# Optimization experiments

Hardware: AMD Instinct MI355X
Metric: run time of the kernel (lower is better)

## Reference

```python
import jax, jax.numpy as jnp
import numpy as np

D = 256          # embed_dim
NS = 400000      # num_symbols
PAD = NS         # padding index
B = 2048         # query batch
FEW = 5          # support set size
K = 64           # max neighbors
DM = 2 * D       # d_model
DI = 2 * DM      # ffn inner dim
H = 2 * DM       # lstm hidden
STEPS = 4        # process_steps
EPS = 1e-3       # LayerNormalization eps


def setup_inputs():
    key = jax.random.key(0)
    ks = jax.random.split(key, 20)
    emb = (jax.random.normal(ks[0], (NS + 1, D), jnp.float32) * 0.02).at[PAD].set(0.0)
    gcn_W = jax.random.normal(ks[1], (D, 2 * D), jnp.float32) * (1.0 / np.sqrt(2 * D))
    gcn_wb = jnp.zeros((D,), jnp.float32)
    gcn_b = jnp.zeros((D,), jnp.float32)
    gate_w = 1.0 + jax.random.normal(ks[2], (NS, 1), jnp.float32) * 0.05
    gate_temp = jnp.asarray(1.0, jnp.float32)
    p1_W = jax.random.normal(ks[3], (DI, DM), jnp.float32) * (1.0 / np.sqrt(DM))
    p1_b = jnp.zeros((DI,), jnp.float32)
    p2_W = jax.random.normal(ks[4], (DM, DI), jnp.float32) * (1.0 / np.sqrt(DI))
    p2_b = jnp.zeros((DM,), jnp.float32)
    ln_a = jnp.ones((DM,), jnp.float32)
    ln_b = jnp.zeros((DM,), jnp.float32)
    W_ih = jax.random.normal(ks[5], (4 * H, DM), jnp.float32) * (1.0 / np.sqrt(DM))
    W_hh = jax.random.normal(ks[6], (4 * H, H), jnp.float32) * (1.0 / np.sqrt(H))
    b_ih = jnp.zeros((4 * H,), jnp.float32)
    b_hh = jnp.zeros((4 * H,), jnp.float32)
    query = jax.random.randint(ks[7], (B, 2), 0, NS)
    support = jax.random.randint(ks[8], (FEW, 2), 0, NS)
    q_l1 = jax.random.randint(ks[9], (B, K, 2), 0, NS)
    q_deg_l = jax.random.randint(ks[10], (B,), 0, K + 1)
    q_r1 = jax.random.randint(ks[11], (B, K, 2), 0, NS)
    q_deg_r = jax.random.randint(ks[12], (B,), 0, K + 1)
    s_l1 = jax.random.randint(ks[13], (FEW, K, 2), 0, NS)
    s_deg_l = jax.random.randint(ks[14], (FEW,), 0, K + 1)
    s_r1 = jax.random.randint(ks[15], (FEW, K, 2), 0, NS)
    s_deg_r = jax.random.randint(ks[16], (FEW,), 0, K + 1)
    return dict(emb=emb, gcn_W=gcn_W, gcn_wb=gcn_wb, gcn_b=gcn_b, gate_w=gate_w,
                gate_temp=gate_temp, p1_W=p1_W, p1_b=p1_b, p2_W=p2_W, p2_b=p2_b,
                ln_a=ln_a, ln_b=ln_b, W_ih=W_ih, W_hh=W_hh, b_ih=b_ih, b_hh=b_hh,
                query=query, support=support, q_l1=q_l1, q_deg_l=q_deg_l,
                q_r1=q_r1, q_deg_r=q_deg_r, s_l1=s_l1, s_deg_l=s_deg_l,
                s_r1=s_r1, s_deg_r=s_deg_r)


def _neighbor_encoder(emb, gcn_W, gcn_wb, gcn_b, gate_w, gate_temp, conn, deg, self_ids):
    rel = conn[:, :, 0]                                       # [N, K]
    ent = conn[:, :, 1]
    cat = jnp.concatenate([emb[rel], emb[ent]], axis=-1)      # [N, K, 2D]
    proj = jax.nn.leaky_relu(jnp.einsum('nkc,dc->nkd', cat, gcn_W) + gcn_wb + gcn_b)
    proj = jnp.where((rel == PAD)[:, :, None], 0.0, proj)     # zero out pad neighbors
    degf = deg.astype(jnp.float32)
    agg = proj.sum(axis=1) / jnp.maximum(degf, 1.0)[:, None]  # masked mean over K
    nrel = jnp.where(rel == PAD, 0, rel)
    gate = jax.nn.sigmoid(gate_w[nrel, 0].mean(axis=1, keepdims=True) / gate_temp)
    gate = jnp.where(degf[:, None] > 0, gate, 1.0)
    return jnp.tanh(emb[self_ids] + gate * agg)               # [N, D]


def _layer_norm(z, a, b):
    mu = z.mean(axis=-1, keepdims=True)
    sigma = jnp.std(z, axis=-1, keepdims=True, ddof=1)        # torch.std is unbiased
    return (z - mu) / (sigma + EPS) * a + b


def _support_encoder(x, p1_W, p1_b, p2_W, p2_b, ln_a, ln_b):
    h = jax.nn.relu(x @ p1_W.T + p1_b)
    return _layer_norm(h @ p2_W.T + p2_b + x, ln_a, ln_b)


def _query_encoder(support, query, W_ih, W_hh, b_ih, b_hh):
    n = query.shape[0]
    h_r = jnp.zeros((n, H), query.dtype)
    c = jnp.zeros((n, H), query.dtype)
    h = query
    for _ in range(STEPS):  # small fixed process-step loop
        gates = query @ W_ih.T + b_ih + h_r @ W_hh.T + b_hh
        i, f, g, o = jnp.split(gates, 4, axis=1)
        c = jax.nn.sigmoid(f) * c + jax.nn.sigmoid(i) * jnp.tanh(g)
        h_new = jax.nn.sigmoid(o) * jnp.tanh(c)
        h = query + h_new[:, :DM]
        attn = jax.nn.softmax(h @ support.T, axis=1)
        h_r = jnp.concatenate([h, attn @ support], axis=1)
    return h


def reference(emb, gcn_W, gcn_wb, gcn_b, gate_w, gate_temp, p1_W, p1_b, p2_W, p2_b,
              ln_a, ln_b, W_ih, W_hh, b_ih, b_hh,
              query, support, q_l1, q_deg_l, q_r1, q_deg_r, s_l1, s_deg_l, s_r1, s_deg_r):
    ne = lambda conn, deg, ids: _neighbor_encoder(emb, gcn_W, gcn_wb, gcn_b, gate_w,
                                                  gate_temp, conn, deg, ids)
    q_vec = jnp.concatenate([ne(q_l1, q_deg_l, query[:, 0]),
                             ne(q_r1, q_deg_r, query[:, 1])], axis=-1)   # [B, 2D]
    s_vec = jnp.concatenate([ne(s_l1, s_deg_l, support[:, 0]),
                             ne(s_r1, s_deg_r, support[:, 1])], axis=-1) # [FEW, 2D]
    s_g = _support_encoder(s_vec, p1_W, p1_b, p2_W, p2_b, ln_a, ln_b).mean(axis=0, keepdims=True)
    q_enc = _support_encoder(q_vec, p1_W, p1_b, p2_W, p2_b, ln_a, ln_b)
    q_g = _query_encoder(s_g, q_enc, W_ih, W_hh, b_ih, b_hh)
    return jnp.sum(q_g * s_g, axis=1)                                     # [B]
```

## Files before the change

kernel.cpp:

```cpp
#include <hip/hip_runtime.h>
#include <math.h>

#define PADID 400000

typedef __attribute__((ext_vector_type(8))) short bf16x8;
typedef __attribute__((ext_vector_type(4))) float f32x4;

__device__ __forceinline__ float sigmoidf_(float x){ return 1.0f/(1.0f+__expf(-x)); }
__device__ __forceinline__ float ftanh(float x){ return 1.0f - 2.0f/(__expf(2.0f*x)+1.0f); }

__device__ __forceinline__ unsigned short f2bf(float f){
    unsigned u = __float_as_uint(f);
    u += 0x7FFFu + ((u >> 16) & 1u);
    return (unsigned short)(u >> 16);
}
__device__ __forceinline__ float bf2f(unsigned short s){
    return __uint_as_float(((unsigned)s) << 16);
}

__device__ __forceinline__ int perm_orig(int mp){
    int gate = (mp >> 4) & 3;
    int j = (mp >> 6) * 16 + (mp & 15);
    return gate * 1024 + j;
}

__global__ __launch_bounds__(256) void preconvert(
    const float* __restrict__ gcnW, const float* __restrict__ p1W,
    const float* __restrict__ p2W, const float* __restrict__ Wih,
    const float* __restrict__ Whh, const float* __restrict__ b_ih,
    const float* __restrict__ b_hh,
    unsigned short* __restrict__ wgcn, unsigned short* __restrict__ p1w,
    unsigned short* __restrict__ p2w, unsigned short* __restrict__ wih_p,
    unsigned short* __restrict__ whh_p, float* __restrict__ bias0_p)
{
    long long i = ((long long)blockIdx.x * 256 + threadIdx.x) * 4;
    float4 v;
    if (i < 131072LL) {
        v = *(const float4*)(gcnW + i);
        unsigned a0 = f2bf(v.x) | ((unsigned)f2bf(v.y) << 16);
        unsigned a1 = f2bf(v.z) | ((unsigned)f2bf(v.w) << 16);
        *(uint2*)(wgcn + i) = make_uint2(a0, a1);
    } else if (i < 655360LL) {
        long long off = i - 131072LL;
        v = *(const float4*)(p1W + off);
        unsigned a0 = f2bf(v.x) | ((unsigned)f2bf(v.y) << 16);
        unsigned a1 = f2bf(v.z) | ((unsigned)f2bf(v.w) << 16);
        *(uint2*)(p1w + off) = make_uint2(a0, a1);
    } else if (i < 1179648LL) {
        long long off = i - 655360LL;
        v = *(const float4*)(p2W + off);
        unsigned a0 = f2bf(v.x) | ((unsigned)f2bf(v.y) << 16);
        unsigned a1 = f2bf(v.z) | ((unsigned)f2bf(v.w) << 16);
        *(uint2*)(p2w + off) = make_uint2(a0, a1);
    } else if (i < 3276800LL) {
        long long off = i - 1179648LL;
        int mp = (int)(off >> 9), col = (int)(off & 511);
        int orig = perm_orig(mp);
        v = *(const float4*)(Wih + (long long)orig * 512 + col);
        unsigned a0 = f2bf(v.x) | ((unsigned)f2bf(v.y) << 16);
        unsigned a1 = f2bf(v.z) | ((unsigned)f2bf(v.w) << 16);
        *(uint2*)(wih_p + off) = make_uint2(a0, a1);
    } else if (i < 5373952LL) {
        long long off = i - 3276800LL;
        int mp = (int)(off >> 9), col = (int)(off & 511);
        int orig = perm_orig(mp);
        v = *(const float4*)(Whh + (long long)orig * 1024 + col);
        unsigned a0 = f2bf(v.x) | ((unsigned)f2bf(v.y) << 16);
        unsigned a1 = f2bf(v.z) | ((unsigned)f2bf(v.w) << 16);
        *(uint2*)(whh_p + off) = make_uint2(a0, a1);
    } else if (i < 5378048LL) {
        long long off = i - 5373952LL;
        #pragma unroll
        for (int q = 0; q < 4; q++) {
            int mp = (int)off + q;
            int orig = perm_orig(mp);
            bias0_p[mp] = b_ih[orig] + b_hh[orig];
        }
    }
}

__device__ __forceinline__ void ne_decode(int s,
    const int* q_l1, const int* q_deg_l, const int* q_r1, const int* q_deg_r,
    const int* s_l1, const int* s_deg_l, const int* s_r1, const int* s_deg_r,
    const int* query, const int* support,
    const int*& conn, const int*& deg, const int*& ids, int& n, int& ids_off, int& row, int& col)
{
    if (s < 2048)      { conn = q_l1; deg = q_deg_l; ids = query;   n = s;      ids_off = 0; row = s;        col = 0;   }
    else if (s < 4096) { conn = q_r1; deg = q_deg_r; ids = query;   n = s-2048; ids_off = 1; row = s-2048;   col = 256; }
    else if (s < 4101) { conn = s_l1; deg = s_deg_l; ids = support; n = s-4096; ids_off = 0; row = 2048+n;   col = 0;   }
    else               { conn = s_r1; deg = s_deg_r; ids = support; n = s-4101; ids_off = 1; row = 2048+n;   col = 256; }
}

__global__ __launch_bounds__(256, 2) void ne_fused(
    const float* __restrict__ emb, const unsigned short* __restrict__ Wbf,
    const float* __restrict__ wb, const float* __restrict__ bb,
    const float* __restrict__ gate_w, const float* __restrict__ gate_temp,
    const int* __restrict__ q_l1, const int* __restrict__ q_deg_l,
    const int* __restrict__ q_r1, const int* __restrict__ q_deg_r,
    const int* __restrict__ s_l1, const int* __restrict__ s_deg_l,
    const int* __restrict__ s_r1, const int* __restrict__ s_deg_r,
    const int* __restrict__ query, const int* __restrict__ support,
    unsigned short* __restrict__ vec_bf)
{
    __shared__ int   rel_s[128];
    __shared__ int   ent_s[128];
    __shared__ unsigned short A_lds[128 * 72];
    __shared__ unsigned short B_lds[256 * 72];
    __shared__ float red[4][4][128];
    __shared__ float gw_s[128];
    __shared__ float gate_sh[2];

    const int bid = blockIdx.x;
    const int t = threadIdx.x;
    const int lane = t & 63, w = t >> 6, lr = lane & 15, kg = lane >> 4;
    const int si_w = w >> 1;
    const int wc0 = (w & 1) * 128;

    {
        int si = t >> 7, u = t & 127;
        const int *conn, *deg, *ids; int n, ids_off, row, col;
        ne_decode(bid*2 + si, q_l1,q_deg_l,q_r1,q_deg_r,s_l1,s_deg_l,s_r1,s_deg_r,
                  query, support, conn, deg, ids, n, ids_off, row, col);
        int v = conn[n*128 + u];
        if (u & 1) ent_s[si*64 + (u>>1)] = v; else rel_s[si*64 + (u>>1)] = v;
    }
    __syncthreads();

    const int rr = t >> 1, half = t & 1;

    float4 a_reg[8];
    #define ISSUE_A(ch_) { \
        const int side_ = ((ch_) >= 4); \
        const int cg0_ = ((ch_) & 3) * 64; \
        int rowid_ = side_ ? ent_s[rr] : rel_s[rr]; \
        const float* src_ = emb + (long long)rowid_ * 256 + cg0_ + half * 32; \
        _Pragma("unroll") \
        for (int q_ = 0; q_ < 8; q_++) a_reg[q_] = *(const float4*)(src_ + q_*4); \
    }

    ISSUE_A(0);

    if (t < 128) {
        int r = rel_s[t];
        gw_s[t] = gate_w[(r == PADID) ? 0 : r];
    }
    __syncthreads();
    if ((t & 63) == 0 && t < 128) {
        int si = t >> 6;
        const int *conn, *deg, *ids; int n, ids_off, row, col;
        ne_decode(bid*2 + si, q_l1,q_deg_l,q_r1,q_deg_r,s_l1,s_deg_l,s_r1,s_deg_r,
                  query, support, conn, deg, ids, n, ids_off, row, col);
        float s = 0.0f;
        for (int k = 0; k < 64; k++) s += gw_s[si*64 + k];
        float g = sigmoidf_((s * (1.0f/64.0f)) / gate_temp[0]);
        if (!((float)deg[n] > 0.0f)) g = 1.0f;
        gate_sh[si] = g;
    }

    f32x4 acc[4][8];
    #pragma unroll
    for (int i = 0; i < 4; i++)
        #pragma unroll
        for (int j = 0; j < 8; j++)
            acc[i][j] = (f32x4){0.f,0.f,0.f,0.f};

    for (int ch = 0; ch < 8; ch++) {
        #pragma unroll
        for (int j = 0; j < 8; j++) {
            int row = j * 32 + (t >> 3);
            bf16x8 v = *(const bf16x8*)(Wbf + (long long)row * 512 + ch*64 + (t & 7) * 8);
            *(bf16x8*)&B_lds[row*72 + (t & 7) * 8] = v;
        }
        {
            unsigned short* dst = &A_lds[rr*72 + half*32];
            #pragma unroll
            for (int q = 0; q < 4; q++) {
                float4 v0 = a_reg[2*q];
                float4 v1 = a_reg[2*q + 1];
                bf16x8 o;
                o[0]=(short)f2bf(v0.x); o[1]=(short)f2bf(v0.y); o[2]=(short)f2bf(v0.z); o[3]=(short)f2bf(v0.w);
                o[4]=(short)f2bf(v1.x); o[5]=(short)f2bf(v1.y); o[6]=(short)f2bf(v1.z); o[7]=(short)f2bf(v1.w);
                *(bf16x8*)(dst + q*8) = o;
            }
        }
        __syncthreads();
        if (ch < 7) ISSUE_A(ch + 1);
        #pragma unroll
        for (int ks = 0; ks < 64; ks += 32) {
            bf16x8 a[4], b[8];
            #pragma unroll
            for (int rt = 0; rt < 4; rt++)
                a[rt] = *(const bf16x8*)&A_lds[(si_w*64 + rt*16 + lr)*72 + ks + kg*8];
            #pragma unroll
            for (int ct = 0; ct < 8; ct++)
                b[ct] = *(const bf16x8*)&B_lds[(wc0 + ct*16 + lr)*72 + ks + kg*8];
            #pragma unroll
            for (int rt = 0; rt < 4; rt++)
                #pragma unroll
                for (int ct = 0; ct < 8; ct++)
                    acc[rt][ct] = __builtin_amdgcn_mfma_f32_16x16x32_bf16(a[rt], b[ct], acc[rt][ct], 0, 0, 0);
        }
        __syncthreads();
    }
    #undef ISSUE_A

    #pragma unroll
    for (int ct = 0; ct < 8; ct++) {
        int d = wc0 + ct*16 + lr;
        float bd = wb[d] + bb[d];
        float pp = 0.0f;
        #pragma unroll
        for (int rt = 0; rt < 4; rt++) {
            int rbase = si_w*64 + rt*16 + kg*4;
            #pragma unroll
            for (int reg = 0; reg < 4; reg++) {
                if (rel_s[rbase + reg] != PADID) {
                    float v = acc[rt][ct][reg] + bd;
                    v = (v > 0.0f) ? v : 0.01f * v;
                    pp += v;
                }
            }
        }
        red[w][kg][ct*16 + lr] = pp;
    }
    __syncthreads();

    #pragma unroll
    for (int si = 0; si < 2; si++) {
        int wv = si*2 + (t >> 7), cl = t & 127;
        float agg = red[wv][0][cl] + red[wv][1][cl] + red[wv][2][cl] + red[wv][3][cl];
        const int *conn, *deg, *ids; int n, ids_off, row, col;
        ne_decode(bid*2 + si, q_l1,q_deg_l,q_r1,q_deg_r,s_l1,s_deg_l,s_r1,s_deg_r,
                  query, support, conn, deg, ids, n, ids_off, row, col);
        float degf = fmaxf((float)deg[n], 1.0f);
        agg /= degf;
        int id = ids[n*2 + ids_off];
        float o = ftanh(emb[(long long)id * 256 + t] + gate_sh[si] * agg);
        vec_bf[(long long)row * 512 + col + t] = f2bf(o);
    }
}

template<int HB, int HADD, int RELU, int WF, int WB>
__global__ __launch_bounds__(256) void mfma_gemm(
    const unsigned short* __restrict__ A, const unsigned short* __restrict__ B,
    const float* __restrict__ bias, const unsigned short* __restrict__ addbf,
    float* __restrict__ Cf, unsigned short* __restrict__ Cb, int N, int M, int K)
{
    __shared__ unsigned short A_lds[128 * 72];
    __shared__ unsigned short B_lds[128 * 72];
    const int t = threadIdx.x;
    const int bm0 = blockIdx.x * 128, bn0 = blockIdx.y * 128;
    const int lane = t & 63, w = t >> 6, wn = w >> 1, wm = w & 1;
    const int lr = lane & 15, kg = lane >> 4;

    f32x4 acc[4][4];
    #pragma unroll
    for (int i = 0; i < 4; i++)
        #pragma unroll
        for (int j = 0; j < 4; j++)
            acc[i][j] = (f32x4){0.f,0.f,0.f,0.f};

    const int r = t >> 1, half = t & 1;
    const unsigned short* Ap = A + (size_t)(bn0 + r) * K + half * 32;
    const unsigned short* Bp = B + (size_t)(bm0 + r) * K + half * 32;
    unsigned short* Aw = &A_lds[r*72 + half*32];
    unsigned short* Bw = &B_lds[r*72 + half*32];

    for (int c0 = 0; c0 < K; c0 += 64) {
        #pragma unroll
        for (int q = 0; q < 4; q++) {
            *(bf16x8*)(Aw + q*8) = *(const bf16x8*)(Ap + c0 + q*8);
            *(bf16x8*)(Bw + q*8) = *(const bf16x8*)(Bp + c0 + q*8);
        }
        __syncthreads();
        #pragma unroll
        for (int ks = 0; ks < 64; ks += 32) {
            bf16x8 a[4], b[4];
            #pragma unroll
            for (int rt = 0; rt < 4; rt++)
                a[rt] = *(const bf16x8*)&A_lds[(wn*64 + rt*16 + lr)*72 + ks + kg*8];
            #pragma unroll
            for (int ct = 0; ct < 4; ct++)
                b[ct] = *(const bf16x8*)&B_lds[(wm*64 + ct*16 + lr)*72 + ks + kg*8];
            #pragma unroll
            for (int rt = 0; rt < 4; rt++)
                #pragma unroll
                for (int ct = 0; ct < 4; ct++)
                    acc[rt][ct] = __builtin_amdgcn_mfma_f32_16x16x32_bf16(a[rt], b[ct], acc[rt][ct], 0, 0, 0);
        }
        __syncthreads();
    }

    float bsum[4];
    #pragma unroll
    for (int ct = 0; ct < 4; ct++)
        bsum[ct] = HB ? bias[bm0 + wm*64 + ct*16 + lr] : 0.0f;
    #pragma unroll
    for (int rt = 0; rt < 4; rt++) {
        #pragma unroll
        for (int reg = 0; reg < 4; reg++) {
            int n = bn0 + wn*64 + rt*16 + kg*4 + reg;
            if (n < N) {
                size_t rowb = (size_t)n * M + bm0 + wm*64;
                #pragma unroll
                for (int ct = 0; ct < 4; ct++) {
                    size_t idx = rowb + ct*16 + lr;
                    float v = acc[rt][ct][reg] + bsum[ct];
                    if (HADD) v += bf2f(addbf[idx]);
                    if (RELU) v = fmaxf(v, 0.0f);
                    if (WF) Cf[idx] = v;
                    if (WB) Cb[idx] = f2bf(v);
                }
            }
        }
    }
}

template<int FIRST>
__global__ __launch_bounds__(256, 2) void lstm_gemm(
    const unsigned short* __restrict__ A, const unsigned short* __restrict__ B,
    const float* __restrict__ biasv, unsigned short* __restrict__ G0,
    float* __restrict__ c_st, const float* __restrict__ qenc,
    unsigned short* __restrict__ h_bf)
{
    __shared__ unsigned short A_lds[128 * 72];
    __shared__ unsigned short B_lds[128 * 72];
    const int t = threadIdx.x;
    const int bm0 = blockIdx.x * 128, bn0 = blockIdx.y * 128;
    const int lane = t & 63, w = t >> 6, wn = w >> 1, wm = w & 1;
    const int lr = lane & 15, kg = lane >> 4;

    f32x4 acc[4][4];
    #pragma unroll
    for (int i = 0; i < 4; i++)
        #pragma unroll
        for (int j = 0; j < 4; j++)
            acc[i][j] = (f32x4){0.f,0.f,0.f,0.f};

    const int r = t >> 1, half = t & 1;
    const unsigned short* Ap = A + (size_t)(bn0 + r) * 512 + half * 32;
    const unsigned short* Bp = B + (size_t)(bm0 + r) * 512 + half * 32;
    unsigned short* Aw = &A_lds[r*72 + half*32];
    unsigned short* Bw = &B_lds[r*72 + half*32];

    for (int c0 = 0; c0 < 512; c0 += 64) {
        #pragma unroll
        for (int q = 0; q < 4; q++) {
            *(bf16x8*)(Aw + q*8) = *(const bf16x8*)(Ap + c0 + q*8);
            *(bf16x8*)(Bw + q*8) = *(const bf16x8*)(Bp + c0 + q*8);
        }
        __syncthreads();
        #pragma unroll
        for (int ks = 0; ks < 64; ks += 32) {
            bf16x8 a[4], b[4];
            #pragma unroll
            for (int rt = 0; rt < 4; rt++)
                a[rt] = *(const bf16x8*)&A_lds[(wn*64 + rt*16 + lr)*72 + ks + kg*8];
            #pragma unroll
            for (int ct = 0; ct < 4; ct++)
                b[ct] = *(const bf16x8*)&B_lds[(wm*64 + ct*16 + lr)*72 + ks + kg*8];
            #pragma unroll
            for (int rt = 0; rt < 4; rt++)
                #pragma unroll
                for (int ct = 0; ct < 4; ct++)
                    acc[rt][ct] = __builtin_amdgcn_mfma_f32_16x16x32_bf16(a[rt], b[ct], acc[rt][ct], 0, 0, 0);
        }
        __syncthreads();
    }

    const int g0col = (bm0 + wm*64) >> 6;
    const int j = g0col*16 + lr;
    float e[4];
    #pragma unroll
    for (int ct = 0; ct < 4; ct++)
        e[ct] = biasv[bm0 + wm*64 + ct*16 + lr];

    #pragma unroll
    for (int rt = 0; rt < 4; rt++) {
        #pragma unroll
        for (int reg = 0; reg < 4; reg++) {
            int n = bn0 + wn*64 + rt*16 + kg*4 + reg;
            size_t gbase = (size_t)n * 4096 + bm0 + wm*64;
            float gi = acc[rt][0][reg] + e[0];
            float gf = acc[rt][1][reg] + e[1];
            float gg = acc[rt][2][reg] + e[2];
            float go = acc[rt][3][reg] + e[3];
            if (FIRST) {
                G0[gbase + 0*16 + lr] = f2bf(gi);
                G0[gbase + 1*16 + lr] = f2bf(gf);
                G0[gbase + 2*16 + lr] = f2bf(gg);
                G0[gbase + 3*16 + lr] = f2bf(go);
            } else {
                gi += bf2f(G0[gbase + 0*16 + lr]);
                gf += bf2f(G0[gbase + 1*16 + lr]);
                gg += bf2f(G0[gbase + 2*16 + lr]);
                go += bf2f(G0[gbase + 3*16 + lr]);
            }
            size_t cidx = (size_t)n * 1024 + j;
            float cprev = FIRST ? 0.0f : c_st[cidx];
            float cv = sigmoidf_(gf) * cprev + sigmoidf_(gi) * ftanh(gg);
            c_st[cidx] = cv;
            float hn = sigmoidf_(go) * ftanh(cv);
            if (j < 512)
                h_bf[(size_t)n * 512 + j] = f2bf(qenc[(size_t)n * 512 + j] + hn);
        }
    }
}

__global__ __launch_bounds__(256) void ln_kernel(
    const float* __restrict__ z, const float* __restrict__ a,
    const float* __restrict__ b, float* __restrict__ o,
    unsigned short* __restrict__ ob)
{
    __shared__ float red[256];
    int n = blockIdx.x, t = threadIdx.x;
    const float* zp = z + (long long)n * 512;
    float2 v = *(const float2*)(zp + t*2);
    red[t] = v.x + v.y;
    __syncthreads();
    for (int off = 128; off > 0; off >>= 1) {
        if (t < off) red[t] += red[t+off];
        __syncthreads();
    }
    float mu = red[0] * (1.0f/512.0f);
    __syncthreads();
    float d0 = v.x - mu, d1 = v.y - mu;
    red[t] = d0*d0 + d1*d1;
    __syncthreads();
    for (int off = 128; off > 0; off >>= 1) {
        if (t < off) red[t] += red[t+off];
        __syncthreads();
    }
    float var = red[0] * (1.0f/511.0f);
    float inv = 1.0f / (sqrtf(var) + 1e-3f);
    float r0 = d0 * inv * a[t*2]   + b[t*2];
    float r1 = d1 * inv * a[t*2+1] + b[t*2+1];
    float* op = o + (long long)n * 512;
    op[t*2] = r0; op[t*2+1] = r1;
    unsigned short* obp = ob + (long long)n * 512;
    obp[t*2] = f2bf(r0); obp[t*2+1] = f2bf(r1);
}

__global__ __launch_bounds__(256) void mean5_kernel(
    const float* __restrict__ se, float* __restrict__ sg)
{
    int d = blockIdx.x * 256 + threadIdx.x;
    if (d < 512) {
        float s = 0.0f;
        #pragma unroll
        for (int f = 0; f < 5; f++) s += se[f*512 + d];
        sg[d] = s * 0.2f;
    }
}

__global__ __launch_bounds__(256) void svecg_kernel(
    const float* __restrict__ sg, const float* __restrict__ Whh,
    float* __restrict__ outv)
{
    __shared__ float sgl[512];
    int t = threadIdx.x;
    sgl[t] = sg[t]; sgl[256+t] = sg[256+t];
    __syncthreads();
    int mp = blockIdx.x * 256 + t;
    int orig = perm_orig(mp);
    const float* wp = Whh + (long long)orig * 1024 + 512;
    float s = 0.0f;
    for (int k = 0; k < 512; k += 4) {
        float4 wv = *(const float4*)(wp + k);
        s += sgl[k]*wv.x + sgl[k+1]*wv.y + sgl[k+2]*wv.z + sgl[k+3]*wv.w;
    }
    outv[mp] = s;
}

__global__ __launch_bounds__(256) void dot_kernel(
    const unsigned short* __restrict__ h_bf, const float* __restrict__ sg,
    float* __restrict__ out)
{
    int w = threadIdx.x >> 6, lane = threadIdx.x & 63;
    int n = blockIdx.x * 4 + w;
    bf16x8 hv = *(const bf16x8*)(h_bf + (long long)n * 512 + lane * 8);
    const float* sp = sg + lane * 8;
    float4 b0 = *(const float4*)sp, b1 = *(const float4*)(sp+4);
    float bs[8] = {b0.x,b0.y,b0.z,b0.w,b1.x,b1.y,b1.z,b1.w};
    float p = 0.0f;
    #pragma unroll
    for (int q = 0; q < 8; q++) p += bf2f((unsigned short)hv[q]) * bs[q];
    #pragma unroll
    for (int off = 32; off > 0; off >>= 1) p += __shfl_down(p, off);
    if (lane == 0) out[n] = p;
}

extern "C" void kernel_launch(void* const* d_in, const int* in_sizes, int n_in,
                              void* d_out, int out_size, void* d_ws, size_t ws_size,
                              hipStream_t stream)
{
    (void)in_sizes; (void)n_in; (void)out_size; (void)ws_size;
    const float* emb       = (const float*)d_in[0];
    const float* gcn_W     = (const float*)d_in[1];
    const float* gcn_wb    = (const float*)d_in[2];
    const float* gcn_b     = (const float*)d_in[3];
    const float* gate_w    = (const float*)d_in[4];
    const float* gate_temp = (const float*)d_in[5];
    const float* p1_W      = (const float*)d_in[6];
    const float* p1_b      = (const float*)d_in[7];
    const float* p2_W      = (const float*)d_in[8];
    const float* p2_b      = (const float*)d_in[9];
    const float* ln_a      = (const float*)d_in[10];
    const float* ln_b      = (const float*)d_in[11];
    const float* W_ih      = (const float*)d_in[12];
    const float* W_hh      = (const float*)d_in[13];
    const float* b_ih      = (const float*)d_in[14];
    const float* b_hh      = (const float*)d_in[15];
    const int*   query     = (const int*)d_in[16];
    const int*   support   = (const int*)d_in[17];
    const int*   q_l1      = (const int*)d_in[18];
    const int*   q_deg_l   = (const int*)d_in[19];
    const int*   q_r1      = (const int*)d_in[20];
    const int*   q_deg_r   = (const int*)d_in[21];
    const int*   s_l1      = (const int*)d_in[22];
    const int*   s_deg_l   = (const int*)d_in[23];
    const int*   s_r1      = (const int*)d_in[24];
    const int*   s_deg_r   = (const int*)d_in[25];
    float* out = (float*)d_out;
    typedef unsigned short us;

    char* wp_ = (char*)d_ws;
    auto take = [&](size_t bytes) { void* p = wp_; wp_ += (bytes + 255) & ~(size_t)255; return p; };
    us*    vec_bf  = (us*)   take((size_t)2176*512*2);
    us*    h1_bf   = (us*)   take((size_t)2176*1024*2);
    float* z_buf   = (float*)take((size_t)2176*512*4);
    float* enc_f   = (float*)take((size_t)2176*512*4);
    us*    enc_bf  = (us*)   take((size_t)2176*512*2);
    float* s_g     = (float*)take(512*4);
    float* bias0_p = (float*)take(4096*4);
    float* svec_p  = (float*)take(4096*4);
    float* c_st    = (float*)take((size_t)2048*1024*4);
    us*    h_bf    = (us*)   take((size_t)2048*512*2);
    us*    wgcn    = (us*)   take((size_t)256*512*2);
    us*    p1w     = (us*)   take((size_t)1024*512*2);
    us*    p2w     = (us*)   take((size_t)512*1024*2);
    us*    wih_p   = (us*)   take((size_t)4096*512*2);
    us*    whh_p   = (us*)   take((size_t)4096*512*2);
    us*    G0_bf   = (us*)   take((size_t)2048*4096*2);

    preconvert<<<5252, 256, 0, stream>>>(gcn_W, p1_W, p2_W, W_ih, W_hh, b_ih, b_hh,
        wgcn, p1w, p2w, wih_p, whh_p, bias0_p);

    ne_fused<<<2053, 256, 0, stream>>>(emb, wgcn, gcn_wb, gcn_b, gate_w, gate_temp,
        q_l1, q_deg_l, q_r1, q_deg_r, s_l1, s_deg_l, s_r1, s_deg_r,
        query, support, vec_bf);

    mfma_gemm<1,0,1,0,1><<<dim3(8,17), 256, 0, stream>>>(vec_bf, p1w, p1_b, nullptr, nullptr, h1_bf, 2053, 1024, 512);
    mfma_gemm<1,1,0,1,0><<<dim3(4,17), 256, 0, stream>>>(h1_bf, p2w, p2_b, vec_bf, z_buf, nullptr, 2053, 512, 1024);
    ln_kernel<<<2053, 256, 0, stream>>>(z_buf, ln_a, ln_b, enc_f, enc_bf);
    mean5_kernel<<<2, 256, 0, stream>>>(enc_f + (size_t)2048*512, s_g);
    svecg_kernel<<<16, 256, 0, stream>>>(s_g, W_hh, svec_p);

    lstm_gemm<1><<<dim3(32,16), 256, 0, stream>>>(enc_bf, wih_p, bias0_p, G0_bf, c_st, enc_f, h_bf);
    for (int s2 = 0; s2 < 3; s2++)
        lstm_gemm<0><<<dim3(32,16), 256, 0, stream>>>(h_bf, whh_p, svec_p, G0_bf, c_st, enc_f, h_bf);

    dot_kernel<<<512, 256, 0, stream>>>(h_bf, s_g, out);
}
```

Before: 888.3 us.

## Split neighbor encoder to one sample per block; trim final LSTM step

The neighbor-encoder kernel now handles one sample per block instead of two: a 64x256 tile, each wave covering 64 output columns, with the gate reduction done by warp shuffles. This removes the shared-memory reduction buffer, cuts accumulator registers and raises the occupancy bound to 3, at the cost of twice as many blocks each reloading the GCN weight tile. The last LSTM step launches a new mode over half the column blocks and skips writing the cell state. Only the first DM hidden columns and no later cell state are needed after that step.

```diff
diff --git a/kernel.cpp b/kernel.cpp
--- a/kernel.cpp
+++ b/kernel.cpp
@@ -91,7 +91,7 @@
     else               { conn = s_r1; deg = s_deg_r; ids = support; n = s-4101; ids_off = 1; row = 2048+n;   col = 256; }
 }
 
-__global__ __launch_bounds__(256, 2) void ne_fused(
+__global__ __launch_bounds__(256, 3) void ne_fused(
     const float* __restrict__ emb, const unsigned short* __restrict__ Wbf,
     const float* __restrict__ wb, const float* __restrict__ bb,
     const float* __restrict__ gate_w, const float* __restrict__ gate_temp,
@@ -102,116 +102,110 @@
     const int* __restrict__ query, const int* __restrict__ support,
     unsigned short* __restrict__ vec_bf)
 {
-    __shared__ int   rel_s[128];
-    __shared__ int   ent_s[128];
-    __shared__ unsigned short A_lds[128 * 72];
+    __shared__ int   rel_s[64];
+    __shared__ int   ent_s[64];
+    __shared__ unsigned short A_lds[64 * 72];
     __shared__ unsigned short B_lds[256 * 72];
-    __shared__ float red[4][4][128];
-    __shared__ float gw_s[128];
-    __shared__ float gate_sh[2];
-
-    const int bid = blockIdx.x;
+    __shared__ float gate_sh;
+
     const int t = threadIdx.x;
     const int lane = t & 63, w = t >> 6, lr = lane & 15, kg = lane >> 4;
-    const int si_w = w >> 1;
-    const int wc0 = (w & 1) * 128;
-
-    {
-        int si = t >> 7, u = t & 127;
-        const int *conn, *deg, *ids; int n, ids_off, row, col;
-        ne_decode(bid*2 + si, q_l1,q_deg_l,q_r1,q_deg_r,s_l1,s_deg_l,s_r1,s_deg_r,
-                  query, support, conn, deg, ids, n, ids_off, row, col);
-        int v = conn[n*128 + u];
-        if (u & 1) ent_s[si*64 + (u>>1)] = v; else rel_s[si*64 + (u>>1)] = v;
+    const int wc0 = w * 64;
+
+    const int *conn, *deg, *ids; int n, ids_off, row, col;
+    ne_decode(blockIdx.x, q_l1,q_deg_l,q_r1,q_deg_r,s_l1,s_deg_l,s_r1,s_deg_r,
+              query, support, conn, deg, ids, n, ids_off, row, col);
+
+    if (t < 128) {
+        int v = conn[n*128 + t];
+        if (t & 1) ent_s[t>>1] = v; else rel_s[t>>1] = v;
     }
     __syncthreads();
 
-    const int rr = t >> 1, half = t & 1;
-
-    float4 a_reg[8];
+    const int arow = t >> 2, aq = t & 3;
+
+    float4 a_reg[4];
     #define ISSUE_A(ch_) { \
         const int side_ = ((ch_) >= 4); \
         const int cg0_ = ((ch_) & 3) * 64; \
-        int rowid_ = side_ ? ent_s[rr] : rel_s[rr]; \
-        const float* src_ = emb + (long long)rowid_ * 256 + cg0_ + half * 32; \
+        int rowid_ = side_ ? ent_s[arow] : rel_s[arow]; \
+        const float* src_ = emb + (long long)rowid_ * 256 + cg0_ + aq * 16; \
         _Pragma("unroll") \
-        for (int q_ = 0; q_ < 8; q_++) a_reg[q_] = *(const float4*)(src_ + q_*4); \
+        for (int q_ = 0; q_ < 4; q_++) a_reg[q_] = *(const float4*)(src_ + q_*4); \
     }
 
     ISSUE_A(0);
 
-    if (t < 128) {
+    if (t < 64) {
         int r = rel_s[t];
-        gw_s[t] = gate_w[(r == PADID) ? 0 : r];
-    }
-    __syncthreads();
-    if ((t & 63) == 0 && t < 128) {
-        int si = t >> 6;
-        const int *conn, *deg, *ids; int n, ids_off, row, col;
-        ne_decode(bid*2 + si, q_l1,q_deg_l,q_r1,q_deg_r,s_l1,s_deg_l,s_r1,s_deg_r,
-                  query, support, conn, deg, ids, n, ids_off, row, col);
-        float s = 0.0f;
-        for (int k = 0; k < 64; k++) s += gw_s[si*64 + k];
-        float g = sigmoidf_((s * (1.0f/64.0f)) / gate_temp[0]);
-        if (!((float)deg[n] > 0.0f)) g = 1.0f;
-        gate_sh[si] = g;
-    }
-
-    f32x4 acc[4][8];
+        float gwv = gate_w[(r == PADID) ? 0 : r];
+        #pragma unroll
+        for (int off = 32; off > 0; off >>= 1) gwv += __shfl_down(gwv, off);
+        if (t == 0) {
+            float g = sigmoidf_((gwv * (1.0f/64.0f)) / gate_temp[0]);
+            if (!((float)deg[n] > 0.0f)) g = 1.0f;
+            gate_sh = g;
+        }
+    }
+
+    f32x4 acc[4][4];
     #pragma unroll
     for (int i = 0; i < 4; i++)
         #pragma unroll
-        for (int j = 0; j < 8; j++)
+        for (int j = 0; j < 4; j++)
             acc[i][j] = (f32x4){0.f,0.f,0.f,0.f};
 
     for (int ch = 0; ch < 8; ch++) {
         #pragma unroll
         for (int j = 0; j < 8; j++) {
-            int row = j * 32 + (t >> 3);
-            bf16x8 v = *(const bf16x8*)(Wbf + (long long)row * 512 + ch*64 + (t & 7) * 8);
-            *(bf16x8*)&B_lds[row*72 + (t & 7) * 8] = v;
+            int brow = j * 32 + (t >> 3);
+            bf16x8 v = *(const bf16x8*)(Wbf + (long long)brow * 512 + ch*64 + (t & 7) * 8);
+            *(bf16x8*)&B_lds[brow*72 + (t & 7) * 8] = v;
         }
         {
-            unsigned short* dst = &A_lds[rr*72 + half*32];
-            #pragma unroll
-            for (int q = 0; q < 4; q++) {
-                float4 v0 = a_reg[2*q];
-                float4 v1 = a_reg[2*q + 1];
-                bf16x8 o;
-                o[0]=(short)f2bf(v0.x); o[1]=(short)f2bf(v0.y); o[2]=(short)f2bf(v0.z); o[3]=(short)f2bf(v0.w);
-                o[4]=(short)f2bf(v1.x); o[5]=(short)f2bf(v1.y); o[6]=(short)f2bf(v1.z); o[7]=(short)f2bf(v1.w);
-                *(bf16x8*)(dst + q*8) = o;
-            }
+            unsigned short* dst = &A_lds[arow*72 + aq*16];
+            bf16x8 o0, o1;
+            o0[0]=(short)f2bf(a_reg[0].x); o0[1]=(short)f2bf(a_reg[0].y);
+            o0[2]=(short)f2bf(a_reg[0].z); o0[3]=(short)f2bf(a_reg[0].w);
+            o0[4]=(short)f2bf(a_reg[1].x); o0[5]=(short)f2bf(a_reg[1].y);
+            o0[6]=(short)f2bf(a_reg[1].z); o0[7]=(short)f2bf(a_reg[1].w);
+            o1[0]=(short)f2bf(a_reg[2].x); o1[1]=(short)f2bf(a_reg[2].y);
+            o1[2]=(short)f2bf(a_reg[2].z); o1[3]=(short)f2bf(a_reg[2].w);
+            o1[4]=(short)f2bf(a_reg[3].x); o1[5]=(short)f2bf(a_reg[3].y);
+            o1[6]=(short)f2bf(a_reg[3].z); o1[7]=(short)f2bf(a_reg[3].w);
+            *(bf16x8*)(dst)     = o0;
+            *(bf16x8*)(dst + 8) = o1;
         }
         __syncthreads();
         if (ch < 7) ISSUE_A(ch + 1);
         #pragma unroll
         for (int ks = 0; ks < 64; ks += 32) {
-            bf16x8 a[4], b[8];
+            bf16x8 a[4], b[4];
             #pragma unroll
             for (int rt = 0; rt < 4; rt++)
-                a[rt] = *(const bf16x8*)&A_lds[(si_w*64 + rt*16 + lr)*72 + ks + kg*8];
-            #pragma unroll
-            for (int ct = 0; ct < 8; ct++)
+                a[rt] = *(const bf16x8*)&A_lds[(rt*16 + lr)*72 + ks + kg*8];
+            #pragma unroll
+            for (int ct = 0; ct < 4; ct++)
                 b[ct] = *(const bf16x8*)&B_lds[(wc0 + ct*16 + lr)*72 + ks + kg*8];
             #pragma unroll
             for (int rt = 0; rt < 4; rt++)
                 #pragma unroll
-                for (int ct = 0; ct < 8; ct++)
+                for (int ct = 0; ct < 4; ct++)
                     acc[rt][ct] = __builtin_amdgcn_mfma_f32_16x16x32_bf16(a[rt], b[ct], acc[rt][ct], 0, 0, 0);
         }
         __syncthreads();
     }
     #undef ISSUE_A
 
-    #pragma unroll
-    for (int ct = 0; ct < 8; ct++) {
+    float outv0, outv1, outv2, outv3;
+    #pragma unroll
+    for (int ct = 0; ct < 4; ct++) {
         int d = wc0 + ct*16 + lr;
         float bd = wb[d] + bb[d];
         float pp = 0.0f;
         #pragma unroll
         for (int rt = 0; rt < 4; rt++) {
-            int rbase = si_w*64 + rt*16 + kg*4;
+            int rbase = rt*16 + kg*4;
             #pragma unroll
             for (int reg = 0; reg < 4; reg++) {
                 if (rel_s[rbase + reg] != PADID) {
@@ -221,23 +215,18 @@
                 }
             }
         }
-        red[w][kg][ct*16 + lr] = pp;
-    }
-    __syncthreads();
-
-    #pragma unroll
-    for (int si = 0; si < 2; si++) {
-        int wv = si*2 + (t >> 7), cl = t & 127;
-        float agg = red[wv][0][cl] + red[wv][1][cl] + red[wv][2][cl] + red[wv][3][cl];
-        const int *conn, *deg, *ids; int n, ids_off, row, col;
-        ne_decode(bid*2 + si, q_l1,q_deg_l,q_r1,q_deg_r,s_l1,s_deg_l,s_r1,s_deg_r,
-                  query, support, conn, deg, ids, n, ids_off, row, col);
-        float degf = fmaxf((float)deg[n], 1.0f);
-        agg /= degf;
-        int id = ids[n*2 + ids_off];
-        float o = ftanh(emb[(long long)id * 256 + t] + gate_sh[si] * agg);
-        vec_bf[(long long)row * 512 + col + t] = f2bf(o);
-    }
+        pp += __shfl_xor(pp, 16);
+        pp += __shfl_xor(pp, 32);
+        if (ct == 0) outv0 = pp; else if (ct == 1) outv1 = pp;
+        else if (ct == 2) outv2 = pp; else outv3 = pp;
+    }
+    float agg = (kg == 0) ? outv0 : (kg == 1) ? outv1 : (kg == 2) ? outv2 : outv3;
+    int dcol = wc0 + kg*16 + lr;
+    float degf = fmaxf((float)deg[n], 1.0f);
+    agg /= degf;
+    int id = ids[n*2 + ids_off];
+    float o = ftanh(emb[(long long)id * 256 + dcol] + gate_sh * agg);
+    vec_bf[(long long)row * 512 + col + dcol] = f2bf(o);
 }
 
 template<int HB, int HADD, int RELU, int WF, int WB>
@@ -316,7 +305,7 @@
     }
 }
 
-template<int FIRST>
+template<int MODE>
 __global__ __launch_bounds__(256, 2) void lstm_gemm(
     const unsigned short* __restrict__ A, const unsigned short* __restrict__ B,
     const float* __restrict__ biasv, unsigned short* __restrict__ G0,
@@ -385,7 +374,7 @@
             float gf = acc[rt][1][reg] + e[1];
             float gg = acc[rt][2][reg] + e[2];
             float go = acc[rt][3][reg] + e[3];
-            if (FIRST) {
+            if (MODE == 1) {
                 G0[gbase + 0*16 + lr] = f2bf(gi);
                 G0[gbase + 1*16 + lr] = f2bf(gf);
                 G0[gbase + 2*16 + lr] = f2bf(gg);
@@ -397,9 +386,9 @@
                 go += bf2f(G0[gbase + 3*16 + lr]);
             }
             size_t cidx = (size_t)n * 1024 + j;
-            float cprev = FIRST ? 0.0f : c_st[cidx];
+            float cprev = (MODE == 1) ? 0.0f : c_st[cidx];
             float cv = sigmoidf_(gf) * cprev + sigmoidf_(gi) * ftanh(gg);
-            c_st[cidx] = cv;
+            if (MODE != 2) c_st[cidx] = cv;
             float hn = sigmoidf_(go) * ftanh(cv);
             if (j < 512)
                 h_bf[(size_t)n * 512 + j] = f2bf(qenc[(size_t)n * 512 + j] + hn);
@@ -546,7 +535,7 @@
     preconvert<<<5252, 256, 0, stream>>>(gcn_W, p1_W, p2_W, W_ih, W_hh, b_ih, b_hh,
         wgcn, p1w, p2w, wih_p, whh_p, bias0_p);
 
-    ne_fused<<<2053, 256, 0, stream>>>(emb, wgcn, gcn_wb, gcn_b, gate_w, gate_temp,
+    ne_fused<<<4106, 256, 0, stream>>>(emb, wgcn, gcn_wb, gcn_b, gate_w, gate_temp,
         q_l1, q_deg_l, q_r1, q_deg_r, s_l1, s_deg_l, s_r1, s_deg_r,
         query, support, vec_bf);
 
@@ -557,8 +546,9 @@
     svecg_kernel<<<16, 256, 0, stream>>>(s_g, W_hh, svec_p);
 
     lstm_gemm<1><<<dim3(32,16), 256, 0, stream>>>(enc_bf, wih_p, bias0_p, G0_bf, c_st, enc_f, h_bf);
-    for (int s2 = 0; s2 < 3; s2++)
+    for (int s2 = 0; s2 < 2; s2++)
         lstm_gemm<0><<<dim3(32,16), 256, 0, stream>>>(h_bf, whh_p, svec_p, G0_bf, c_st, enc_f, h_bf);
+    lstm_gemm<2><<<dim3(16,16), 256, 0, stream>>>(h_bf, whh_p, svec_p, G0_bf, c_st, enc_f, h_bf);
 
     dot_kernel<<<512, 256, 0, stream>>>(h_bf, s_g, out);
 }
```

Measured after the change: 846.4 us. -4.7%, faster.
